# Kernel optimization log

Hardware: AMD Instinct MI355X
Metric: run time of the kernel (lower is better)

Reference implementation:

```python
import jax, jax.numpy as jnp
import numpy as np

KM_ITERS = 25  # fixed Lloyd iterations (original kmeans_pytorch iterates to tol; fixed count for jit)
EPS = 1e-12    # torch F.normalize clamp_min eps


def l2_normalize(x):
    n = jnp.sqrt(jnp.sum(x * x, axis=1, keepdims=True))
    return x / jnp.maximum(n, EPS)


def kmeans(X, k, iters=KM_ITERS):
    """Lloyd's algorithm, euclidean distance, deterministic init from first k rows."""
    N = X.shape[0]
    centers0 = X[:k]
    xsq = jnp.sum(X * X, axis=1, keepdims=True)  # [N,1]

    def dist2(centers):
        # squared euclidean distances [N,k]; argmin identical to euclidean
        return xsq - 2.0 * (X @ centers.T) + jnp.sum(centers * centers, axis=1)

    def step(i, centers):
        lab = jnp.argmin(dist2(centers), axis=1)  # [N]
        sums = jax.ops.segment_sum(X, lab, num_segments=k)  # [k,d]
        cnts = jax.ops.segment_sum(jnp.ones((N,), X.dtype), lab, num_segments=k)  # [k]
        new = sums / jnp.maximum(cnts, 1.0)[:, None]
        # keep old center for empty clusters
        return jnp.where(cnts[:, None] > 0, new, centers)

    centers = jax.lax.fori_loop(0, iters, step, centers0)
    labels = jnp.argmin(dist2(centers), axis=1)
    return labels, centers


def setup_inputs() -> dict:
    key = jax.random.key(0)
    ks = jax.random.split(key, 8)
    N, D, H, K = 50000, 1024, 512, 64
    x = jax.random.normal(ks[0], (N, D), dtype=jnp.float32)
    xw = jax.random.normal(ks[1], (N, D), dtype=jnp.float32)
    s1 = 1.0 / np.sqrt(D)
    s2 = 1.0 / np.sqrt(H)
    W1 = jax.random.uniform(ks[2], (D, H), jnp.float32, -s1, s1)
    b1 = jax.random.uniform(ks[3], (H,), jnp.float32, -s1, s1)
    W2 = jax.random.uniform(ks[4], (D, H), jnp.float32, -s1, s1)
    b2 = jax.random.uniform(ks[5], (H,), jnp.float32, -s1, s1)
    Wc = jax.random.uniform(ks[6], (H, K), jnp.float32, -s2, s2)
    bc = jax.random.uniform(ks[7], (K,), jnp.float32, -s2, s2)
    return {"x": x, "xw": xw, "W1": W1, "b1": b1, "W2": W2, "b2": b2,
            "Wc": Wc, "bc": bc, "n_clusters": K}


def reference(x, xw, W1, b1, W2, b2, Wc, bc, n_clusters):
    out1 = l2_normalize(x @ W1 + b1)   # layers1 + F.normalize(dim=1)
    out2 = l2_normalize(xw @ W2 + b2)  # layers2 + F.normalize(dim=1)
    # kmeans results are detached in the original (converted to numpy)
    km_label, km_centers = kmeans(jax.lax.stop_gradient(out2), n_clusters)
    u1 = jax.nn.softmax(out1 @ Wc + bc, axis=1)
    u2 = jax.nn.softmax(out2 @ Wc + bc, axis=1)
    return (out1, out2, km_label, km_centers, u1, u2)
```

## Files before the change

kernel.cpp:

```cpp
#include <hip/hip_runtime.h>
#include <math.h>

#define ND 1024
#define HID 512
#define KCL 64
#define KM_ITERS 25
#define CHSZ 256


__device__ __forceinline__ float np_pw512_sq(const float* __restrict__ a, int lane)
{
#pragma clang fp contract(off)
  float r = 0.f;
  if (lane < 32) {
    const float* blk = a + 128 * (lane >> 3);
    int j = lane & 7;
    float t = blk[j];
    r = t * t;
#pragma unroll
    for (int i = 8; i < 128; i += 8) { float u = blk[j + i]; r = r + u * u; }
  }
  float t1 = r  + __shfl_xor(r,  1);
  float t2 = t1 + __shfl_xor(t1, 2);
  float t3 = t2 + __shfl_xor(t2, 4);
  float u4 = t3 + __shfl_xor(t3, 8);
  float v5 = u4 + __shfl_xor(u4, 16);
  return __shfl(v5, 0);
}

__global__ __launch_bounds__(512) void np_gemm2_kernel(
    const float* __restrict__ A, const float* __restrict__ W,
    const float* __restrict__ bias, float* __restrict__ C)
{
#pragma clang fp contract(off)
  __shared__ float4 As4[8 * 256];
  const int t = threadIdx.x;
  const int r0 = blockIdx.x * 8;
  const float4* Ag = (const float4*)(A + (size_t)r0 * ND);
  for (int i = t; i < 8 * 256; i += 512) As4[i] = Ag[i];
  __syncthreads();

  float a0[8], a1[8], a2[8], a3[8];
#pragma unroll
  for (int r = 0; r < 8; r++) { a0[r] = 0.f; a1[r] = 0.f; a2[r] = 0.f; a3[r] = 0.f; }

#define G2_STEP(ACC, K4)                                          \
  {                                                               \
    int k = (K4) * 4;                                             \
    float w0 = W[(size_t)(k + 0) * HID + t];                      \
    float w1 = W[(size_t)(k + 1) * HID + t];                      \
    float w2 = W[(size_t)(k + 2) * HID + t];                      \
    float w3 = W[(size_t)(k + 3) * HID + t];                      \
    _Pragma("unroll")                                             \
    for (int r = 0; r < 8; r++) {                                 \
      float4 a = As4[r * 256 + (K4)];                             \
      float s = ACC[r];                                           \
      s = fmaf(a.x, w0, s);                                       \
      s = fmaf(a.y, w1, s);                                       \
      s = fmaf(a.z, w2, s);                                       \
      s = fmaf(a.w, w3, s);                                       \
      ACC[r] = s;                                                 \
    }                                                             \
  }

#pragma unroll 4
  for (int k4 = 0; k4 < 80; k4++)    G2_STEP(a0, k4)
#pragma unroll 4
  for (int k4 = 80; k4 < 160; k4++)  G2_STEP(a1, k4)
#pragma unroll 4
  for (int k4 = 160; k4 < 208; k4++) G2_STEP(a2, k4)
#pragma unroll 4
  for (int k4 = 208; k4 < 256; k4++) G2_STEP(a3, k4)
#undef G2_STEP

  float b = bias[t];
#pragma unroll
  for (int r = 0; r < 8; r++)
    C[(size_t)(r0 + r) * HID + t] = (((a0[r] + a1[r]) + a2[r]) + a3[r]) + b;
}

__global__ __launch_bounds__(256) void np_rownorm_xsq_kernel(
    float* __restrict__ M, float* __restrict__ xsq, int N)
{
#pragma clang fp contract(off)
  __shared__ float sy[4][512];
  int w = threadIdx.x >> 6, lane = threadIdx.x & 63;
  int r = blockIdx.x * 4 + w;
  if (r >= N) return;
  float* row = M + (size_t)r * HID;
  float s = np_pw512_sq(row, lane);
  float n = fmaxf((float)sqrt((double)s), 1e-12f);
#pragma unroll
  for (int j = 0; j < 8; j++) {
    float y = row[lane * 8 + j] / n;
    row[lane * 8 + j] = y;
    sy[w][lane * 8 + j] = y;
  }
  __syncthreads();
  float s2 = np_pw512_sq(sy[w], lane);
  if (lane == 0) xsq[r] = s2;
}

__global__ __launch_bounds__(64) void np_csqT_kernel(
    const float* __restrict__ cen, float* __restrict__ csq, float* __restrict__ Ct)
{
#pragma clang fp contract(off)
  int c = blockIdx.x;
  int lane = threadIdx.x;
  const float* row = cen + (size_t)c * HID;
  float s = np_pw512_sq(row, lane);
  if (lane == 0) csq[c] = s;
  for (int k = lane; k < HID; k += 64) Ct[(size_t)k * KCL + c] = row[k];
}

__global__ __launch_bounds__(256) void np_label_kernel(
    const float* __restrict__ X, const float* __restrict__ Ct,
    const float* __restrict__ xsq, const float* __restrict__ csq,
    int* __restrict__ lab, int N)
{
#pragma clang fp contract(off)
  __shared__ float Xs[16][512];
  const int t = threadIdx.x;
  const int p0 = blockIdx.x * 16;
  const float4* Xg = (const float4*)(X + (size_t)p0 * HID);
  float4* Xs4 = (float4*)&Xs[0][0];
  for (int i = t; i < 16 * 128; i += 256) Xs4[i] = Xg[i];
  __syncthreads();

  const int w = t >> 6, c = t & 63;
  const int pl = w * 4;
  float s0[4], s1[4];
#pragma unroll
  for (int pt = 0; pt < 4; pt++) { s0[pt] = 0.f; s1[pt] = 0.f; }

#pragma unroll 8
  for (int k = 0; k < 256; k++) {
    float ct = Ct[(size_t)k * KCL + c];
#pragma unroll
    for (int pt = 0; pt < 4; pt++) s0[pt] = fmaf(Xs[pl + pt][k], ct, s0[pt]);
  }
#pragma unroll 8
  for (int k = 256; k < 512; k++) {
    float ct = Ct[(size_t)k * KCL + c];
#pragma unroll
    for (int pt = 0; pt < 4; pt++) s1[pt] = fmaf(Xs[pl + pt][k], ct, s1[pt]);
  }

#pragma unroll
  for (int pt = 0; pt < 4; pt++) {
    int p = p0 + pl + pt;
    float dot = s0[pt] + s1[pt];
    float t2 = 2.0f * dot;
    float u = xsq[p] - t2;
    float sc = u + csq[c];
    float bv = sc; int bi = c;
#pragma unroll
    for (int m = 32; m; m >>= 1) {
      float ov = __shfl_xor(bv, m);
      int   oi = __shfl_xor(bi, m);
      if (ov < bv || (ov == bv && oi < bi)) { bv = ov; bi = oi; }
    }
    if (c == 0 && p < N) lab[p] = bi;
  }
}


__global__ __launch_bounds__(256) void k_count(
    const int* __restrict__ lab, int* __restrict__ cntch, int N)
{
  int ch = blockIdx.x;
  int p = ch * CHSZ + threadIdx.x;
  int l = (p < N) ? lab[p] : -1;
  int w = threadIdx.x >> 6, lane = threadIdx.x & 63;
  __shared__ int wc[4][64];
  for (int cc = 0; cc < 64; cc++) {
    unsigned long long mm = __ballot(l == cc);
    if (lane == cc) wc[w][cc] = __popcll(mm);
  }
  __syncthreads();
  if (threadIdx.x < 64) {
    int cc = threadIdx.x;
    cntch[ch * 64 + cc] = wc[0][cc] + wc[1][cc] + wc[2][cc] + wc[3][cc];
  }
}

__global__ __launch_bounds__(64) void k_prefix(
    const int* __restrict__ cntch, int* __restrict__ off,
    int* __restrict__ base, int* __restrict__ cnt, int CH)
{
  int c = threadIdx.x;
  int run = 0;
  for (int ch = 0; ch < CH; ch++) { off[ch * 64 + c] = run; run += cntch[ch * 64 + c]; }
  cnt[c] = run;
  __shared__ int tot[64];
  tot[c] = run;
  __syncthreads();
  if (c == 0) {
    int b = 0;
    for (int cc = 0; cc < 64; cc++) { base[cc] = b; b += tot[cc]; }
  }
  __syncthreads();
  int b = base[c];
  for (int ch = 0; ch < CH; ch++) off[ch * 64 + c] += b;
}

__global__ __launch_bounds__(256) void k_scatter(
    const int* __restrict__ lab, const int* __restrict__ off,
    int* __restrict__ list, int N)
{
  int ch = blockIdx.x;
  int p = ch * CHSZ + threadIdx.x;
  int l = (p < N) ? lab[p] : -1;
  int w = threadIdx.x >> 6, lane = threadIdx.x & 63;
  __shared__ int wc[4][64];
  int rank = 0;
  for (int cc = 0; cc < 64; cc++) {
    unsigned long long mm = __ballot(l == cc);
    if (lane == cc) wc[w][cc] = __popcll(mm);
    if (l == cc) rank = __popcll(mm & ((1ull << lane) - 1ull));
  }
  __syncthreads();
  if (p < N) {
    int before = 0;
    for (int ww = 0; ww < 4; ww++) if (ww < w) before += wc[ww][l];
    list[off[ch * 64 + l] + before + rank] = p;
  }
}

__global__ __launch_bounds__(512) void np_seg_kernel(
    const float* __restrict__ X, const int* __restrict__ list,
    const int* __restrict__ base, const int* __restrict__ cnt,
    float* __restrict__ sums)
{
#pragma clang fp contract(off)
  const int c = blockIdx.x;
  const int d = threadIdx.x;
  const int n = cnt[c];
  const int* lp = list + base[c];
  float s = 0.f;
  int i = 0;
  for (; i + 8 <= n; i += 8) {
    int p0 = lp[i + 0], p1 = lp[i + 1], p2 = lp[i + 2], p3 = lp[i + 3];
    int p4 = lp[i + 4], p5 = lp[i + 5], p6 = lp[i + 6], p7 = lp[i + 7];
    float x0 = X[(size_t)p0 * HID + d];
    float x1 = X[(size_t)p1 * HID + d];
    float x2 = X[(size_t)p2 * HID + d];
    float x3 = X[(size_t)p3 * HID + d];
    float x4 = X[(size_t)p4 * HID + d];
    float x5 = X[(size_t)p5 * HID + d];
    float x6 = X[(size_t)p6 * HID + d];
    float x7 = X[(size_t)p7 * HID + d];
    s = s + x0; s = s + x1; s = s + x2; s = s + x3;
    s = s + x4; s = s + x5; s = s + x6; s = s + x7;
  }
  for (; i < n; i++) s = s + X[(size_t)lp[i] * HID + d];
  sums[(size_t)c * HID + d] = s;
}

__global__ __launch_bounds__(512) void np_update_kernel(
    const float* __restrict__ sums, const int* __restrict__ cnt,
    float* __restrict__ cen)
{
#pragma clang fp contract(off)
  int c = blockIdx.x, d = threadIdx.x;
  int n = cnt[c];
  if (n > 0) {
    float cf = (float)n;
    cen[(size_t)c * HID + d] = sums[(size_t)c * HID + d] / fmaxf(cf, 1.0f);
  }
}

__global__ void copy_f32_kernel(const float* __restrict__ s, float* __restrict__ d, int n)
{
  int i = blockIdx.x * blockDim.x + threadIdx.x;
  if (i < n) d[i] = s[i];
}
__global__ void lab_to_f32_kernel(const int* __restrict__ s, float* __restrict__ d, int n)
{
  int i = blockIdx.x * blockDim.x + threadIdx.x;
  if (i < n) d[i] = (float)s[i];
}


__global__ __launch_bounds__(256) void gemm_bias_kernel(
    const float* __restrict__ A, const float* __restrict__ W,
    const float* __restrict__ bias, float* __restrict__ C, int N)
{
  __shared__ alignas(16) float As[16][68];
  __shared__ alignas(16) float Bs[16][68];
  const int t = threadIdx.x;
  const int bm = blockIdx.x * 64;
  const int bn = blockIdx.y * 64;
  const int tn = t & 15;
  const int tm = t >> 4;
  const int la_m = t >> 2;
  const int la_k = (t & 3) * 4;
  int arow = bm + la_m; if (arow >= N) arow = N - 1;
  const int lb_k = t >> 4;
  const int lb_n = (t & 15) * 4;

  float acc[4][4];
#pragma unroll
  for (int i = 0; i < 4; i++)
#pragma unroll
    for (int j = 0; j < 4; j++) acc[i][j] = 0.f;

  for (int k0 = 0; k0 < ND; k0 += 16) {
    float4 av = *reinterpret_cast<const float4*>(&A[(size_t)arow * ND + k0 + la_k]);
    float4 bv = *reinterpret_cast<const float4*>(&W[(size_t)(k0 + lb_k) * HID + bn + lb_n]);
    __syncthreads();
    As[la_k + 0][la_m] = av.x;
    As[la_k + 1][la_m] = av.y;
    As[la_k + 2][la_m] = av.z;
    As[la_k + 3][la_m] = av.w;
    *reinterpret_cast<float4*>(&Bs[lb_k][lb_n]) = bv;
    __syncthreads();
#pragma unroll
    for (int kk = 0; kk < 16; kk++) {
      float4 a4 = *reinterpret_cast<const float4*>(&As[kk][tm * 4]);
      float4 b4 = *reinterpret_cast<const float4*>(&Bs[kk][tn * 4]);
      float ar[4] = {a4.x, a4.y, a4.z, a4.w};
      float br[4] = {b4.x, b4.y, b4.z, b4.w};
#pragma unroll
      for (int i = 0; i < 4; i++)
#pragma unroll
        for (int j = 0; j < 4; j++)
          acc[i][j] = fmaf(ar[i], br[j], acc[i][j]);
    }
  }
  float4 b4 = *reinterpret_cast<const float4*>(&bias[bn + tn * 4]);
#pragma unroll
  for (int i = 0; i < 4; i++) {
    int row = bm + tm * 4 + i;
    if (row < N) {
      float4 o;
      o.x = acc[i][0] + b4.x; o.y = acc[i][1] + b4.y;
      o.z = acc[i][2] + b4.z; o.w = acc[i][3] + b4.w;
      *reinterpret_cast<float4*>(&C[(size_t)row * HID + bn + tn * 4]) = o;
    }
  }
}

__global__ __launch_bounds__(256) void rownorm_kernel(float* __restrict__ M, int N)
{
  int r = blockIdx.x * 4 + (threadIdx.x >> 6);
  int lane = threadIdx.x & 63;
  if (r >= N) return;
  float* row = M + (size_t)r * HID;
  float4 v0 = *reinterpret_cast<const float4*>(&row[lane * 8]);
  float4 v1 = *reinterpret_cast<const float4*>(&row[lane * 8 + 4]);
  float s = v0.x*v0.x + v0.y*v0.y + v0.z*v0.z + v0.w*v0.w
          + v1.x*v1.x + v1.y*v1.y + v1.z*v1.z + v1.w*v1.w;
#pragma unroll
  for (int off = 32; off; off >>= 1) s += __shfl_xor(s, off);
  float nrm = fmaxf(sqrtf(s), 1e-12f);
  v0.x /= nrm; v0.y /= nrm; v0.z /= nrm; v0.w /= nrm;
  v1.x /= nrm; v1.y /= nrm; v1.z /= nrm; v1.w /= nrm;
  *reinterpret_cast<float4*>(&row[lane * 8]) = v0;
  *reinterpret_cast<float4*>(&row[lane * 8 + 4]) = v1;
}

__global__ __launch_bounds__(256) void clf_softmax_kernel(
    const float* __restrict__ X, const float* __restrict__ W,
    const float* __restrict__ bias, float* __restrict__ U, int N)
{
  int p = blockIdx.x * 4 + (threadIdx.x >> 6);
  int c = threadIdx.x & 63;
  if (p >= N) return;
  const float* xr = X + (size_t)p * HID;
  float acc = 0.f;
  for (int d = 0; d < HID; d++) acc = fmaf(xr[d], W[(size_t)d * KCL + c], acc);
  float l = acc + bias[c];
  float mx = l;
#pragma unroll
  for (int m = 32; m; m >>= 1) mx = fmaxf(mx, __shfl_xor(mx, m));
  float e = expf(l - mx);
  float s = e;
#pragma unroll
  for (int m = 32; m; m >>= 1) s += __shfl_xor(s, m);
  U[(size_t)p * KCL + c] = e / s;
}

extern "C" void kernel_launch(void* const* d_in, const int* in_sizes, int n_in,
                              void* d_out, int out_size, void* d_ws, size_t ws_size,
                              hipStream_t stream)
{
  const float* x  = (const float*)d_in[0];
  const float* xw = (const float*)d_in[1];
  const float* W1 = (const float*)d_in[2];
  const float* b1 = (const float*)d_in[3];
  const float* W2 = (const float*)d_in[4];
  const float* b2 = (const float*)d_in[5];
  const float* Wc = (const float*)d_in[6];
  const float* bc = (const float*)d_in[7];

  const int N = in_sizes[0] / ND;
  float* out  = (float*)d_out;
  float* out1 = out;
  float* out2 = out1 + (size_t)N * HID;
  float* labf = out2 + (size_t)N * HID;
  float* cenf = labf + N;
  float* u1   = cenf + (size_t)KCL * HID;
  float* u2   = u1 + (size_t)N * KCL;

  const int CH = (N + CHSZ - 1) / CHSZ;

  float* cen   = u2;
  float* Ct    = cen + KCL * HID;
  float* csq   = Ct + KCL * HID;
  float* sums  = csq + KCL;
  float* xsq   = sums + KCL * HID;
  int*   cnt   = (int*)(xsq + N);
  int*   lab   = cnt + KCL;
  int*   list  = lab + N;
  int*   cntch = list + N;
  int*   off   = cntch + CH * 64;
  int*   base  = off + CH * 64;

  const int mblocks = (N + 63) / 64;
  const int pblocks = (N + 3) / 4;
  const int lblocks = (N + 15) / 16;

  np_gemm2_kernel<<<N / 8, 512, 0, stream>>>(xw, W2, b2, out2);
  np_rownorm_xsq_kernel<<<pblocks, 256, 0, stream>>>(out2, xsq, N);
  copy_f32_kernel<<<(KCL * HID + 255) / 256, 256, 0, stream>>>(out2, cen, KCL * HID);

  for (int it = 0; it < KM_ITERS; ++it) {
    np_csqT_kernel<<<KCL, 64, 0, stream>>>(cen, csq, Ct);
    np_label_kernel<<<lblocks, 256, 0, stream>>>(out2, Ct, xsq, csq, lab, N);
    k_count<<<CH, 256, 0, stream>>>(lab, cntch, N);
    k_prefix<<<1, 64, 0, stream>>>(cntch, off, base, cnt, CH);
    k_scatter<<<CH, 256, 0, stream>>>(lab, off, list, N);
    np_seg_kernel<<<KCL, 512, 0, stream>>>(out2, list, base, cnt, sums);
    np_update_kernel<<<KCL, 512, 0, stream>>>(sums, cnt, cen);
  }
  np_csqT_kernel<<<KCL, 64, 0, stream>>>(cen, csq, Ct);
  np_label_kernel<<<lblocks, 256, 0, stream>>>(out2, Ct, xsq, csq, lab, N);

  lab_to_f32_kernel<<<(N + 255) / 256, 256, 0, stream>>>(lab, labf, N);
  copy_f32_kernel<<<(KCL * HID + 255) / 256, 256, 0, stream>>>(cen, cenf, KCL * HID);

  gemm_bias_kernel<<<dim3(mblocks, HID / 64), 256, 0, stream>>>(x, W1, b1, out1, N);
  rownorm_kernel<<<pblocks, 256, 0, stream>>>(out1, N);
  clf_softmax_kernel<<<pblocks, 256, 0, stream>>>(out1, Wc, bc, u1, N);
  clf_softmax_kernel<<<pblocks, 256, 0, stream>>>(out2, Wc, bc, u2, N);
}
```

Before: 8.771 ms.

## Drop LDS staging in gemm/label kernels, fuse center update with csqT, reuse gemm2

The row-block GEMM and the k-means label kernel now read activation rows straight from global memory with float4 loads instead of staging them in shared memory. The label kernel handles 32 points per block with 8 per wave. The segment-sum kernel is split across two blocks per cluster, and the center update is fused with the squared-norm and transpose computation, which removes one launch per iteration. The separate tiled out1 GEMM is replaced by the same row-block gemm2 kernel. Redundant global loads of the same row across lanes depend on caching, and out1 now uses a different accumulation order.

Measured after the change: 12.71 ms. 44.9% more time.

```diff
diff --git a/kernel.cpp b/kernel.cpp
--- a/kernel.cpp
+++ b/kernel.cpp
@@ -33,50 +33,46 @@
     const float* __restrict__ bias, float* __restrict__ C)
 {
 #pragma clang fp contract(off)
-  __shared__ float4 As4[8 * 256];
   const int t = threadIdx.x;
-  const int r0 = blockIdx.x * 8;
-  const float4* Ag = (const float4*)(A + (size_t)r0 * ND);
-  for (int i = t; i < 8 * 256; i += 512) As4[i] = Ag[i];
-  __syncthreads();
-
-  float a0[8], a1[8], a2[8], a3[8];
-#pragma unroll
-  for (int r = 0; r < 8; r++) { a0[r] = 0.f; a1[r] = 0.f; a2[r] = 0.f; a3[r] = 0.f; }
-
-#define G2_STEP(ACC, K4)                                          \
-  {                                                               \
-    int k = (K4) * 4;                                             \
-    float w0 = W[(size_t)(k + 0) * HID + t];                      \
-    float w1 = W[(size_t)(k + 1) * HID + t];                      \
-    float w2 = W[(size_t)(k + 2) * HID + t];                      \
-    float w3 = W[(size_t)(k + 3) * HID + t];                      \
-    _Pragma("unroll")                                             \
-    for (int r = 0; r < 8; r++) {                                 \
-      float4 a = As4[r * 256 + (K4)];                             \
-      float s = ACC[r];                                           \
-      s = fmaf(a.x, w0, s);                                       \
-      s = fmaf(a.y, w1, s);                                       \
-      s = fmaf(a.z, w2, s);                                       \
-      s = fmaf(a.w, w3, s);                                       \
-      ACC[r] = s;                                                 \
-    }                                                             \
-  }
-
-#pragma unroll 4
-  for (int k4 = 0; k4 < 80; k4++)    G2_STEP(a0, k4)
-#pragma unroll 4
-  for (int k4 = 80; k4 < 160; k4++)  G2_STEP(a1, k4)
-#pragma unroll 4
-  for (int k4 = 160; k4 < 208; k4++) G2_STEP(a2, k4)
-#pragma unroll 4
-  for (int k4 = 208; k4 < 256; k4++) G2_STEP(a3, k4)
+  const size_t r0 = (size_t)blockIdx.x * 8;
+  const float* a0p = A + r0 * ND;
+  float s1[8], s2[8], s3[8], s4[8];
+#pragma unroll
+  for (int r = 0; r < 8; r++) { s1[r] = 0.f; s2[r] = 0.f; s3[r] = 0.f; s4[r] = 0.f; }
+
+#define G2_STEP(ACC, K4)                                                       \
+  {                                                                            \
+    const int k = (K4) * 4;                                                    \
+    float w0 = W[(size_t)(k + 0) * HID + t];                                   \
+    float w1 = W[(size_t)(k + 1) * HID + t];                                   \
+    float w2 = W[(size_t)(k + 2) * HID + t];                                   \
+    float w3 = W[(size_t)(k + 3) * HID + t];                                   \
+    _Pragma("unroll")                                                          \
+    for (int r = 0; r < 8; r++) {                                              \
+      float4 a = *reinterpret_cast<const float4*>(a0p + (size_t)r * ND + k);   \
+      float s = ACC[r];                                                        \
+      s = fmaf(a.x, w0, s);                                                    \
+      s = fmaf(a.y, w1, s);                                                    \
+      s = fmaf(a.z, w2, s);                                                    \
+      s = fmaf(a.w, w3, s);                                                    \
+      ACC[r] = s;                                                              \
+    }                                                                          \
+  }
+
+#pragma unroll 2
+  for (int k4 = 0; k4 < 80; k4++)    G2_STEP(s1, k4)
+#pragma unroll 2
+  for (int k4 = 80; k4 < 160; k4++)  G2_STEP(s2, k4)
+#pragma unroll 2
+  for (int k4 = 160; k4 < 208; k4++) G2_STEP(s3, k4)
+#pragma unroll 2
+  for (int k4 = 208; k4 < 256; k4++) G2_STEP(s4, k4)
 #undef G2_STEP
 
   float b = bias[t];
 #pragma unroll
   for (int r = 0; r < 8; r++)
-    C[(size_t)(r0 + r) * HID + t] = (((a0[r] + a1[r]) + a2[r]) + a3[r]) + b;
+    C[(r0 + r) * HID + t] = (((s1[r] + s2[r]) + s3[r]) + s4[r]) + b;
 }
 
 __global__ __launch_bounds__(256) void np_rownorm_xsq_kernel(
@@ -119,39 +115,50 @@
     int* __restrict__ lab, int N)
 {
 #pragma clang fp contract(off)
-  __shared__ float Xs[16][512];
-  const int t = threadIdx.x;
-  const int p0 = blockIdx.x * 16;
-  const float4* Xg = (const float4*)(X + (size_t)p0 * HID);
-  float4* Xs4 = (float4*)&Xs[0][0];
-  for (int i = t; i < 16 * 128; i += 256) Xs4[i] = Xg[i];
-  __syncthreads();
-
-  const int w = t >> 6, c = t & 63;
-  const int pl = w * 4;
-  float s0[4], s1[4];
-#pragma unroll
-  for (int pt = 0; pt < 4; pt++) { s0[pt] = 0.f; s1[pt] = 0.f; }
-
-#pragma unroll 8
-  for (int k = 0; k < 256; k++) {
-    float ct = Ct[(size_t)k * KCL + c];
-#pragma unroll
-    for (int pt = 0; pt < 4; pt++) s0[pt] = fmaf(Xs[pl + pt][k], ct, s0[pt]);
-  }
-#pragma unroll 8
-  for (int k = 256; k < 512; k++) {
-    float ct = Ct[(size_t)k * KCL + c];
-#pragma unroll
-    for (int pt = 0; pt < 4; pt++) s1[pt] = fmaf(Xs[pl + pt][k], ct, s1[pt]);
-  }
-
-#pragma unroll
-  for (int pt = 0; pt < 4; pt++) {
-    int p = p0 + pl + pt;
+  const int w = threadIdx.x >> 6, c = threadIdx.x & 63;
+  const int p0 = blockIdx.x * 32 + w * 8;
+  const float* xb[8];
+#pragma unroll
+  for (int pt = 0; pt < 8; pt++) {
+    int p = p0 + pt; if (p >= N) p = N - 1;
+    xb[pt] = X + (size_t)p * HID;
+  }
+  float s0[8], s1[8];
+#pragma unroll
+  for (int pt = 0; pt < 8; pt++) { s0[pt] = 0.f; s1[pt] = 0.f; }
+
+#define LB_STEP(ACC, K4)                                                       \
+  {                                                                            \
+    const int k = (K4) * 4;                                                    \
+    float c0 = Ct[(size_t)(k + 0) * KCL + c];                                  \
+    float c1 = Ct[(size_t)(k + 1) * KCL + c];                                  \
+    float c2 = Ct[(size_t)(k + 2) * KCL + c];                                  \
+    float c3 = Ct[(size_t)(k + 3) * KCL + c];                                  \
+    _Pragma("unroll")                                                          \
+    for (int pt = 0; pt < 8; pt++) {                                           \
+      float4 xq = *reinterpret_cast<const float4*>(xb[pt] + k);                \
+      float s = ACC[pt];                                                       \
+      s = fmaf(xq.x, c0, s);                                                   \
+      s = fmaf(xq.y, c1, s);                                                   \
+      s = fmaf(xq.z, c2, s);                                                   \
+      s = fmaf(xq.w, c3, s);                                                   \
+      ACC[pt] = s;                                                             \
+    }                                                                          \
+  }
+
+#pragma unroll 2
+  for (int k4 = 0; k4 < 64; k4++)   LB_STEP(s0, k4)
+#pragma unroll 2
+  for (int k4 = 64; k4 < 128; k4++) LB_STEP(s1, k4)
+#undef LB_STEP
+
+#pragma unroll
+  for (int pt = 0; pt < 8; pt++) {
+    int p = p0 + pt;
+    int pc = (p < N) ? p : N - 1;
     float dot = s0[pt] + s1[pt];
     float t2 = 2.0f * dot;
-    float u = xsq[p] - t2;
+    float u = xsq[pc] - t2;
     float sc = u + csq[c];
     float bv = sc; int bi = c;
 #pragma unroll
@@ -227,14 +234,14 @@
   }
 }
 
-__global__ __launch_bounds__(512) void np_seg_kernel(
+__global__ __launch_bounds__(256) void np_seg_kernel(
     const float* __restrict__ X, const int* __restrict__ list,
     const int* __restrict__ base, const int* __restrict__ cnt,
     float* __restrict__ sums)
 {
 #pragma clang fp contract(off)
   const int c = blockIdx.x;
-  const int d = threadIdx.x;
+  const int d = blockIdx.y * 256 + threadIdx.x;
   const int n = cnt[c];
   const int* lp = list + base[c];
   float s = 0.f;
@@ -257,17 +264,28 @@
   sums[(size_t)c * HID + d] = s;
 }
 
-__global__ __launch_bounds__(512) void np_update_kernel(
+__global__ __launch_bounds__(512) void np_update_csqT_kernel(
     const float* __restrict__ sums, const int* __restrict__ cnt,
-    float* __restrict__ cen)
-{
-#pragma clang fp contract(off)
-  int c = blockIdx.x, d = threadIdx.x;
-  int n = cnt[c];
+    float* __restrict__ cen, float* __restrict__ csq, float* __restrict__ Ct)
+{
+#pragma clang fp contract(off)
+  __shared__ float row[512];
+  const int c = blockIdx.x, d = threadIdx.x;
+  const int n = cnt[c];
+  float v;
   if (n > 0) {
-    float cf = (float)n;
-    cen[(size_t)c * HID + d] = sums[(size_t)c * HID + d] / fmaxf(cf, 1.0f);
-  }
+    v = sums[(size_t)c * HID + d] / fmaxf((float)n, 1.0f);
+    cen[(size_t)c * HID + d] = v;
+  } else {
+    v = cen[(size_t)c * HID + d];
+  }
+  row[d] = v;
+  __syncthreads();
+  if (d < 64) {
+    float s = np_pw512_sq(row, d);
+    if (d == 0) csq[c] = s;
+  }
+  Ct[(size_t)d * KCL + c] = v;
 }
 
 __global__ void copy_f32_kernel(const float* __restrict__ s, float* __restrict__ d, int n)
@@ -281,65 +299,6 @@
   if (i < n) d[i] = (float)s[i];
 }
 
-
-__global__ __launch_bounds__(256) void gemm_bias_kernel(
-    const float* __restrict__ A, const float* __restrict__ W,
-    const float* __restrict__ bias, float* __restrict__ C, int N)
-{
-  __shared__ alignas(16) float As[16][68];
-  __shared__ alignas(16) float Bs[16][68];
-  const int t = threadIdx.x;
-  const int bm = blockIdx.x * 64;
-  const int bn = blockIdx.y * 64;
-  const int tn = t & 15;
-  const int tm = t >> 4;
-  const int la_m = t >> 2;
-  const int la_k = (t & 3) * 4;
-  int arow = bm + la_m; if (arow >= N) arow = N - 1;
-  const int lb_k = t >> 4;
-  const int lb_n = (t & 15) * 4;
-
-  float acc[4][4];
-#pragma unroll
-  for (int i = 0; i < 4; i++)
-#pragma unroll
-    for (int j = 0; j < 4; j++) acc[i][j] = 0.f;
-
-  for (int k0 = 0; k0 < ND; k0 += 16) {
-    float4 av = *reinterpret_cast<const float4*>(&A[(size_t)arow * ND + k0 + la_k]);
-    float4 bv = *reinterpret_cast<const float4*>(&W[(size_t)(k0 + lb_k) * HID + bn + lb_n]);
-    __syncthreads();
-    As[la_k + 0][la_m] = av.x;
-    As[la_k + 1][la_m] = av.y;
-    As[la_k + 2][la_m] = av.z;
-    As[la_k + 3][la_m] = av.w;
-    *reinterpret_cast<float4*>(&Bs[lb_k][lb_n]) = bv;
-    __syncthreads();
-#pragma unroll
-    for (int kk = 0; kk < 16; kk++) {
-      float4 a4 = *reinterpret_cast<const float4*>(&As[kk][tm * 4]);
-      float4 b4 = *reinterpret_cast<const float4*>(&Bs[kk][tn * 4]);
-      float ar[4] = {a4.x, a4.y, a4.z, a4.w};
-      float br[4] = {b4.x, b4.y, b4.z, b4.w};
-#pragma unroll
-      for (int i = 0; i < 4; i++)
-#pragma unroll
-        for (int j = 0; j < 4; j++)
-          acc[i][j] = fmaf(ar[i], br[j], acc[i][j]);
-    }
-  }
-  float4 b4 = *reinterpret_cast<const float4*>(&bias[bn + tn * 4]);
-#pragma unroll
-  for (int i = 0; i < 4; i++) {
-    int row = bm + tm * 4 + i;
-    if (row < N) {
-      float4 o;
-      o.x = acc[i][0] + b4.x; o.y = acc[i][1] + b4.y;
-      o.z = acc[i][2] + b4.z; o.w = acc[i][3] + b4.w;
-      *reinterpret_cast<float4*>(&C[(size_t)row * HID + bn + tn * 4]) = o;
-    }
-  }
-}
 
 __global__ __launch_bounds__(256) void rownorm_kernel(float* __restrict__ M, int N)
 {
@@ -417,30 +376,28 @@
   int*   off   = cntch + CH * 64;
   int*   base  = off + CH * 64;
 
-  const int mblocks = (N + 63) / 64;
   const int pblocks = (N + 3) / 4;
-  const int lblocks = (N + 15) / 16;
+  const int lblocks = (N + 31) / 32;
 
   np_gemm2_kernel<<<N / 8, 512, 0, stream>>>(xw, W2, b2, out2);
   np_rownorm_xsq_kernel<<<pblocks, 256, 0, stream>>>(out2, xsq, N);
   copy_f32_kernel<<<(KCL * HID + 255) / 256, 256, 0, stream>>>(out2, cen, KCL * HID);
+  np_csqT_kernel<<<KCL, 64, 0, stream>>>(cen, csq, Ct);
 
   for (int it = 0; it < KM_ITERS; ++it) {
-    np_csqT_kernel<<<KCL, 64, 0, stream>>>(cen, csq, Ct);
     np_label_kernel<<<lblocks, 256, 0, stream>>>(out2, Ct, xsq, csq, lab, N);
     k_count<<<CH, 256, 0, stream>>>(lab, cntch, N);
     k_prefix<<<1, 64, 0, stream>>>(cntch, off, base, cnt, CH);
     k_scatter<<<CH, 256, 0, stream>>>(lab, off, list, N);
-    np_seg_kernel<<<KCL, 512, 0, stream>>>(out2, list, base, cnt, sums);
-    np_update_kernel<<<KCL, 512, 0, stream>>>(sums, cnt, cen);
-  }
-  np_csqT_kernel<<<KCL, 64, 0, stream>>>(cen, csq, Ct);
+    np_seg_kernel<<<dim3(KCL, 2), 256, 0, stream>>>(out2, list, base, cnt, sums);
+    np_update_csqT_kernel<<<KCL, 512, 0, stream>>>(sums, cnt, cen, csq, Ct);
+  }
   np_label_kernel<<<lblocks, 256, 0, stream>>>(out2, Ct, xsq, csq, lab, N);
 
   lab_to_f32_kernel<<<(N + 255) / 256, 256, 0, stream>>>(lab, labf, N);
   copy_f32_kernel<<<(KCL * HID + 255) / 256, 256, 0, stream>>>(cen, cenf, KCL * HID);
 
-  gemm_bias_kernel<<<dim3(mblocks, HID / 64), 256, 0, stream>>>(x, W1, b1, out1, N);
+  np_gemm2_kernel<<<N / 8, 512, 0, stream>>>(x, W1, b1, out1);
   rownorm_kernel<<<pblocks, 256, 0, stream>>>(out1, N);
   clf_softmax_kernel<<<pblocks, 256, 0, stream>>>(out1, Wc, bc, u1, N);
   clf_softmax_kernel<<<pblocks, 256, 0, stream>>>(out2, Wc, bc, u2, N);
```
